# Optimization experiments

Measured on AMD Instinct MI355X. Metric: run time of the kernel, lower is better.

Reference implementation:

```python
import jax, jax.numpy as jnp
import numpy as np

N_NODES = 100000
N_EDGES = 640000
D_IN = 128
D_OUT = 128


def setup_inputs() -> dict:
    key = jax.random.key(0)
    k1, k2, k3, k4, k5 = jax.random.split(key, 5)
    feats = jax.random.normal(k1, (N_NODES, D_IN), dtype=jnp.float32)
    src = jax.random.randint(k2, (N_EDGES,), 0, N_NODES, dtype=jnp.int32)
    dst = jax.random.randint(k3, (N_EDGES,), 0, N_NODES, dtype=jnp.int32)
    # Xavier-normal-ish init (gain for relu = sqrt(2))
    std = float(np.sqrt(2.0) * np.sqrt(2.0 / (D_IN + D_OUT)))
    linear_skip_weight = jax.random.normal(k4, (D_OUT, D_IN), dtype=jnp.float32) * std
    linear_msg_weight = jax.random.normal(k5, (D_OUT, D_IN), dtype=jnp.float32) * std
    linear_skip_bias = jnp.zeros((D_OUT,), dtype=jnp.float32)
    linear_msg_bias = jnp.zeros((D_OUT,), dtype=jnp.float32)
    return {
        "feats": feats,
        "src": src,
        "dst": dst,
        "linear_skip_weight": linear_skip_weight,
        "linear_skip_bias": linear_skip_bias,
        "linear_msg_weight": linear_msg_weight,
        "linear_msg_bias": linear_msg_bias,
    }


def reference(feats, src, dst, linear_skip_weight, linear_skip_bias,
              linear_msg_weight, linear_msg_bias):
    n = feats.shape[0]
    # degree from scatter-add of edge weights (ones) at source rows
    deg = jax.ops.segment_sum(jnp.ones_like(src, dtype=feats.dtype), src,
                              num_segments=n)
    deg_inv_sqrt = jnp.where(deg > 0, jax.lax.rsqrt(jnp.maximum(deg, 1.0)) * (deg > 0), 0.0)
    deg_inv_sqrt = jnp.where(deg > 0, deg ** -0.5, 0.0)
    # normalize source features, gather along edges, scatter-sum to dst
    feat_src = feats * deg_inv_sqrt[:, None]           # [N, D_IN]
    msgs = feat_src[src]                               # [E, D_IN]
    rst = jax.ops.segment_sum(msgs, dst, num_segments=n)  # [N, D_IN]
    rst = rst * deg_inv_sqrt[:, None]
    rst_ = rst @ linear_msg_weight.T + linear_msg_bias
    skip_x = feats @ linear_skip_weight.T + linear_skip_bias
    return rst_ + skip_x
```

## Files before the change

kernel.cpp:

```cpp
#include <hip/hip_runtime.h>

#define N_NODES 100000
#define N_EDGES 640000
#define D 128
#define NB ((N_NODES + 1023) / 1024)

typedef short v8s __attribute__((ext_vector_type(8)));
typedef float v4f __attribute__((ext_vector_type(4)));

__device__ __forceinline__ unsigned short f2bf(float x) {
    unsigned int u = __builtin_bit_cast(unsigned int, x);
    u += 0x7fffu + ((u >> 16) & 1u);
    return (unsigned short)(u >> 16);
}
__device__ __forceinline__ float bf2f(unsigned int hi) {
    return __builtin_bit_cast(float, hi << 16);
}

__global__ __launch_bounds__(256) void k_zero(int4* __restrict__ pk4) {
    int i = blockIdx.x * blockDim.x + threadIdx.x;
    if (i < N_NODES / 4) pk4[i] = make_int4(0, 0, 0, 0);
}

__global__ __launch_bounds__(256) void k_pre(const float* __restrict__ feats,
                                             const float* __restrict__ Wm,
                                             const float* __restrict__ Ws,
                                             const float* __restrict__ bmsg,
                                             const float* __restrict__ bskip,
                                             const int* __restrict__ src,
                                             const int* __restrict__ dst,
                                             unsigned int* __restrict__ pk,
                                             unsigned short* __restrict__ Bcat,
                                             float* __restrict__ bias,
                                             char* __restrict__ outb) {
    int i = blockIdx.x * blockDim.x + threadIdx.x;
    if (i < D * D) {
        int j = i >> 7;
        int k = i & 127;
        Bcat[j * 256 + k]       = f2bf(Wm[i]);
        Bcat[j * 256 + 128 + k] = f2bf(Ws[i]);
    }
    if (i < D) bias[i] = bmsg[i] + bskip[i];
    if (i < N_EDGES) {
        atomicAdd(&pk[src[i]], 1u);
        atomicAdd(&pk[dst[i]], 0x10000u);
    }
    int g = i * 8;
    int row = g >> 7;
    int col = g & 127;
    if (row < N_NODES) {
        const float4* s = (const float4*)(feats + g);
        float4 x = s[0], y = s[1];
        uint4 p;
        p.x = (unsigned)f2bf(x.x) | ((unsigned)f2bf(x.y) << 16);
        p.y = (unsigned)f2bf(x.z) | ((unsigned)f2bf(x.w) << 16);
        p.z = (unsigned)f2bf(y.x) | ((unsigned)f2bf(y.y) << 16);
        p.w = (unsigned)f2bf(y.z) | ((unsigned)f2bf(y.w) << 16);
        *(uint4*)(outb + (size_t)row * 512 + 256 + col * 2) = p;
    }
}

__global__ __launch_bounds__(256) void k_scan1(const unsigned int* __restrict__ pk,
                                               int* __restrict__ rowptr,
                                               int* __restrict__ bsums) {
    __shared__ int sd[256];
    int t = threadIdx.x;
    int i0 = blockIdx.x * 1024 + t * 4;
    int v[4];
    int s = 0;
#pragma unroll
    for (int q = 0; q < 4; q++) {
        int i = i0 + q;
        v[q] = (i < N_NODES) ? (int)(pk[i] >> 16) : 0;
        s += v[q];
    }
    sd[t] = s;
    __syncthreads();
    for (int off = 1; off < 256; off <<= 1) {
        int y = (t >= off) ? sd[t - off] : 0;
        __syncthreads();
        sd[t] += y;
        __syncthreads();
    }
    int run = sd[t] - s;
    if (t == 255) bsums[blockIdx.x] = sd[255];
#pragma unroll
    for (int q = 0; q < 4; q++) {
        int i = i0 + q;
        if (i < N_NODES) rowptr[i] = run;
        run += v[q];
    }
}

__global__ __launch_bounds__(128) void k_scan2(int* __restrict__ bsums) {
    __shared__ int sd[128];
    int t = threadIdx.x;
    int v = (t < NB) ? bsums[t] : 0;
    sd[t] = v;
    __syncthreads();
    for (int off = 1; off < 128; off <<= 1) {
        int y = (t >= off) ? sd[t - off] : 0;
        __syncthreads();
        sd[t] += y;
        __syncthreads();
    }
    if (t < NB) bsums[t] = sd[t] - v;
}

__global__ __launch_bounds__(256) void k_scan3(const int* __restrict__ bsums,
                                               int* __restrict__ rowptr,
                                               const unsigned int* __restrict__ pk,
                                               float* __restrict__ dis) {
    int add = bsums[blockIdx.x];
    int i0 = blockIdx.x * 1024 + threadIdx.x * 4;
#pragma unroll
    for (int q = 0; q < 4; q++) {
        int i = i0 + q;
        if (i < N_NODES) {
            rowptr[i] += add;
            int d = (int)(pk[i] & 0xffffu);
            dis[i] = (d > 0) ? (1.0f / sqrtf((float)d)) : 0.0f;
        }
    }
}

__global__ __launch_bounds__(256) void k_fill(const int* __restrict__ src,
                                              const int* __restrict__ dst,
                                              int* __restrict__ rowptr,
                                              int* __restrict__ csr_src) {
    int e = blockIdx.x * blockDim.x + threadIdx.x;
    if (e < N_EDGES) {
        int p = atomicAdd(&rowptr[dst[e]], 1);
        csr_src[p] = src[e];
    }
}

__global__ __launch_bounds__(256) void k_agg(char* __restrict__ outb,
                                             const int* __restrict__ rowptr,
                                             const int* __restrict__ csr_src,
                                             const float* __restrict__ dis) {
    int wid = (int)((blockIdx.x * (unsigned)blockDim.x + threadIdx.x) >> 6);
    int lane = threadIdx.x & 63;
    if (wid >= N_NODES) return;
    int grp = lane >> 4;
    int sub = lane & 15;
    int start = (wid == 0) ? 0 : rowptr[wid - 1];
    int end = rowptr[wid];
    float acc[8];
#pragma unroll
    for (int i = 0; i < 8; i++) acc[i] = 0.f;

    for (int base = start; base < end; base += 4) {
        int e = base + grp;
        if (e < end) {
            int s = csr_src[e];
            float sc = dis[s];
            uint4 v = *(const uint4*)(outb + (size_t)s * 512 + 256 + sub * 16);
            acc[0] += bf2f(v.x & 0xffffu) * sc;
            acc[1] += bf2f(v.x >> 16) * sc;
            acc[2] += bf2f(v.y & 0xffffu) * sc;
            acc[3] += bf2f(v.y >> 16) * sc;
            acc[4] += bf2f(v.z & 0xffffu) * sc;
            acc[5] += bf2f(v.z >> 16) * sc;
            acc[6] += bf2f(v.w & 0xffffu) * sc;
            acc[7] += bf2f(v.w >> 16) * sc;
        }
    }
#pragma unroll
    for (int i = 0; i < 8; i++) {
        acc[i] += __shfl_xor(acc[i], 16);
        acc[i] += __shfl_xor(acc[i], 32);
    }
    if (grp == 0) {
        float scn = dis[wid];
        uint4 p;
        p.x = (unsigned)f2bf(acc[0] * scn) | ((unsigned)f2bf(acc[1] * scn) << 16);
        p.y = (unsigned)f2bf(acc[2] * scn) | ((unsigned)f2bf(acc[3] * scn) << 16);
        p.z = (unsigned)f2bf(acc[4] * scn) | ((unsigned)f2bf(acc[5] * scn) << 16);
        p.w = (unsigned)f2bf(acc[6] * scn) | ((unsigned)f2bf(acc[7] * scn) << 16);
        *(uint4*)(outb + (size_t)wid * 512 + sub * 16) = p;
    }
}

__global__ __launch_bounds__(256) void k_gemm(const unsigned short* __restrict__ Bcat,
                                              const float* __restrict__ bias,
                                              float* __restrict__ outf) {
    __shared__ unsigned short Bl[128][264];
    const char* Ab = (const char*)outf;
    int tid = threadIdx.x;
    int lane = tid & 63;
    int w = tid >> 6;
    int n0 = blockIdx.x * 128;

    for (int i = tid; i < 128 * 32; i += 256) {
        int r = i >> 5, c = i & 31;
        *(uint4*)(&Bl[r][c * 8]) = *(const uint4*)(Bcat + r * 256 + c * 8);
    }
    __syncthreads();

    int q = lane >> 4;
    int lr = lane & 15;

    int r0 = n0 + w * 32 + lr;      if (r0 > N_NODES - 1) r0 = N_NODES - 1;
    int r1 = n0 + w * 32 + 16 + lr; if (r1 > N_NODES - 1) r1 = N_NODES - 1;
    const char* a0p = Ab + (size_t)r0 * 512 + q * 16;
    const char* a1p = Ab + (size_t)r1 * 512 + q * 16;

    v4f acc[2][8];
#pragma unroll
    for (int mt = 0; mt < 2; mt++)
#pragma unroll
        for (int t = 0; t < 8; t++) acc[mt][t] = (v4f){0.f, 0.f, 0.f, 0.f};

#pragma unroll
    for (int kk = 0; kk < 8; kk++) {
        v8s a0 = *(const v8s*)(a0p + kk * 64);
        v8s a1 = *(const v8s*)(a1p + kk * 64);
#pragma unroll
        for (int t = 0; t < 8; t++) {
            v8s b = *(const v8s*)(&Bl[t * 16 + lr][kk * 32 + q * 8]);
            acc[0][t] = __builtin_amdgcn_mfma_f32_16x16x32_bf16(a0, b, acc[0][t], 0, 0, 0);
            acc[1][t] = __builtin_amdgcn_mfma_f32_16x16x32_bf16(a1, b, acc[1][t], 0, 0, 0);
        }
    }

#pragma unroll
    for (int t = 0; t < 8; t++) {
        float bv = bias[t * 16 + lr];
#pragma unroll
        for (int mt = 0; mt < 2; mt++) {
            int rowb = n0 + w * 32 + mt * 16 + q * 4;
#pragma unroll
            for (int r = 0; r < 4; r++) {
                int row = rowb + r;
                if (row < N_NODES)
                    outf[(size_t)row * 128 + t * 16 + lr] = acc[mt][t][r] + bv;
            }
        }
    }
}

extern "C" void kernel_launch(void* const* d_in, const int* in_sizes, int n_in,
                              void* d_out, int out_size, void* d_ws, size_t ws_size,
                              hipStream_t stream) {
    const float* feats = (const float*)d_in[0];
    const int*   src   = (const int*)d_in[1];
    const int*   dst   = (const int*)d_in[2];
    const float* Wskip = (const float*)d_in[3];
    const float* bskip = (const float*)d_in[4];
    const float* Wmsg  = (const float*)d_in[5];
    const float* bmsg  = (const float*)d_in[6];

    char* w = (char*)d_ws;
    unsigned int*   pk      = (unsigned int*)w;
    float*          dis     = (float*)(w + 400000);
    int*            rowptr  = (int*)(w + 800000);
    int*            bsums   = (int*)(w + 1200128);
    unsigned short* Bcat    = (unsigned short*)(w + 1200640);
    float*          bias    = (float*)(w + 1266176);
    int*            csr_src = (int*)(w + 1266688);

    hipLaunchKernelGGL(k_zero, dim3((N_NODES / 4 + 255) / 256), dim3(256), 0, stream,
                       (int4*)pk);
    hipLaunchKernelGGL(k_pre, dim3((N_NODES * (D / 8) + 255) / 256), dim3(256), 0,
                       stream, feats, Wmsg, Wskip, bmsg, bskip, src, dst, pk, Bcat,
                       bias, (char*)d_out);
    hipLaunchKernelGGL(k_scan1, dim3(NB), dim3(256), 0, stream, pk, rowptr, bsums);
    hipLaunchKernelGGL(k_scan2, dim3(1), dim3(128), 0, stream, bsums);
    hipLaunchKernelGGL(k_scan3, dim3(NB), dim3(256), 0, stream, bsums, rowptr,
                       pk, dis);
    hipLaunchKernelGGL(k_fill, dim3((N_EDGES + 255) / 256), dim3(256), 0, stream,
                       src, dst, rowptr, csr_src);
    hipLaunchKernelGGL(k_agg, dim3((N_NODES * 64 + 255) / 256), dim3(256), 0, stream,
                       (char*)d_out, rowptr, csr_src, dis);
    hipLaunchKernelGGL(k_gemm, dim3((N_NODES + 127) / 128), dim3(256), 0, stream,
                       Bcat, bias, (float*)d_out);
}
```

Measured before the change: 277.4 us.

## Replace CSR build with fixed-capacity per-node buckets filled during degree counting

When the workspace is large enough, the kernel fills a 16-slot per-destination bucket during the same atomic pass that counts degrees. Edges past 16 slots go to a global overflow list. This drops the three scan kernels and the CSR fill kernel. The source normalisation is computed on the fly with rsqrt of the packed degree instead of a precomputed array. The trade-offs: bucket writes are scattered, high-degree nodes scan the whole overflow list, and results silently drop edges if overflow exceeds the fixed cap.

```diff
diff --git a/kernel.cpp b/kernel.cpp
--- a/kernel.cpp
+++ b/kernel.cpp
@@ -4,6 +4,8 @@
 #define N_EDGES 640000
 #define D 128
 #define NB ((N_NODES + 1023) / 1024)
+#define BKT_C 16
+#define OVF_CAP 32768
 
 typedef short v8s __attribute__((ext_vector_type(8)));
 typedef float v4f __attribute__((ext_vector_type(4)));
@@ -17,9 +19,11 @@
     return __builtin_bit_cast(float, hi << 16);
 }
 
-__global__ __launch_bounds__(256) void k_zero(int4* __restrict__ pk4) {
+__global__ __launch_bounds__(256) void k_zero(int4* __restrict__ pk4,
+                                              int* __restrict__ ovf_cnt) {
     int i = blockIdx.x * blockDim.x + threadIdx.x;
     if (i < N_NODES / 4) pk4[i] = make_int4(0, 0, 0, 0);
+    if (i == 0) *ovf_cnt = 0;
 }
 
 __global__ __launch_bounds__(256) void k_pre(const float* __restrict__ feats,
@@ -32,7 +36,10 @@
                                              unsigned int* __restrict__ pk,
                                              unsigned short* __restrict__ Bcat,
                                              float* __restrict__ bias,
-                                             char* __restrict__ outb) {
+                                             char* __restrict__ outb,
+                                             int* __restrict__ bucket,
+                                             int* __restrict__ ovf_cnt,
+                                             int2* __restrict__ ovf) {
     int i = blockIdx.x * blockDim.x + threadIdx.x;
     if (i < D * D) {
         int j = i >> 7;
@@ -42,15 +49,26 @@
     }
     if (i < D) bias[i] = bmsg[i] + bskip[i];
     if (i < N_EDGES) {
-        atomicAdd(&pk[src[i]], 1u);
-        atomicAdd(&pk[dst[i]], 0x10000u);
+        int s = src[i];
+        int d = dst[i];
+        atomicAdd(&pk[s], 1u);
+        unsigned int old = atomicAdd(&pk[d], 0x10000u);
+        if (bucket) {
+            unsigned int p = old >> 16;
+            if (p < BKT_C) {
+                bucket[d * BKT_C + (int)p] = s;
+            } else {
+                int q = atomicAdd(ovf_cnt, 1);
+                if (q < OVF_CAP) ovf[q] = make_int2(d, s);
+            }
+        }
     }
     int g = i * 8;
     int row = g >> 7;
     int col = g & 127;
     if (row < N_NODES) {
-        const float4* s = (const float4*)(feats + g);
-        float4 x = s[0], y = s[1];
+        const float4* sp = (const float4*)(feats + g);
+        float4 x = sp[0], y = sp[1];
         uint4 p;
         p.x = (unsigned)f2bf(x.x) | ((unsigned)f2bf(x.y) << 16);
         p.y = (unsigned)f2bf(x.z) | ((unsigned)f2bf(x.w) << 16);
@@ -108,19 +126,13 @@
 }
 
 __global__ __launch_bounds__(256) void k_scan3(const int* __restrict__ bsums,
-                                               int* __restrict__ rowptr,
-                                               const unsigned int* __restrict__ pk,
-                                               float* __restrict__ dis) {
+                                               int* __restrict__ rowptr) {
     int add = bsums[blockIdx.x];
     int i0 = blockIdx.x * 1024 + threadIdx.x * 4;
 #pragma unroll
     for (int q = 0; q < 4; q++) {
         int i = i0 + q;
-        if (i < N_NODES) {
-            rowptr[i] += add;
-            int d = (int)(pk[i] & 0xffffu);
-            dis[i] = (d > 0) ? (1.0f / sqrtf((float)d)) : 0.0f;
-        }
+        if (i < N_NODES) rowptr[i] += add;
     }
 }
 
@@ -135,10 +147,78 @@
     }
 }
 
-__global__ __launch_bounds__(256) void k_agg(char* __restrict__ outb,
-                                             const int* __restrict__ rowptr,
-                                             const int* __restrict__ csr_src,
-                                             const float* __restrict__ dis) {
+__device__ __forceinline__ void agg_edge(const char* outb,
+                                         const unsigned int* pk,
+                                         int s, int sub, float* acc) {
+    float sc = rsqrtf((float)(pk[s] & 0xffffu));
+    uint4 v = *(const uint4*)(outb + (size_t)s * 512 + 256 + sub * 16);
+    acc[0] += bf2f(v.x & 0xffffu) * sc;
+    acc[1] += bf2f(v.x >> 16) * sc;
+    acc[2] += bf2f(v.y & 0xffffu) * sc;
+    acc[3] += bf2f(v.y >> 16) * sc;
+    acc[4] += bf2f(v.z & 0xffffu) * sc;
+    acc[5] += bf2f(v.z >> 16) * sc;
+    acc[6] += bf2f(v.w & 0xffffu) * sc;
+    acc[7] += bf2f(v.w >> 16) * sc;
+}
+
+__device__ __forceinline__ void agg_finish(char* outb, int wid,
+                                           unsigned int pkn, int grp, int sub,
+                                           float* acc) {
+#pragma unroll
+    for (int i = 0; i < 8; i++) {
+        acc[i] += __shfl_xor(acc[i], 16);
+        acc[i] += __shfl_xor(acc[i], 32);
+    }
+    if (grp == 0) {
+        int dsrc = (int)(pkn & 0xffffu);
+        float scn = (dsrc > 0) ? rsqrtf((float)dsrc) : 0.0f;
+        uint4 p;
+        p.x = (unsigned)f2bf(acc[0] * scn) | ((unsigned)f2bf(acc[1] * scn) << 16);
+        p.y = (unsigned)f2bf(acc[2] * scn) | ((unsigned)f2bf(acc[3] * scn) << 16);
+        p.z = (unsigned)f2bf(acc[4] * scn) | ((unsigned)f2bf(acc[5] * scn) << 16);
+        p.w = (unsigned)f2bf(acc[6] * scn) | ((unsigned)f2bf(acc[7] * scn) << 16);
+        *(uint4*)(outb + (size_t)wid * 512 + sub * 16) = p;
+    }
+}
+
+__global__ __launch_bounds__(256) void k_agg_bkt(char* __restrict__ outb,
+                                                 const unsigned int* __restrict__ pk,
+                                                 const int* __restrict__ bucket,
+                                                 const int* __restrict__ ovf_cnt,
+                                                 const int2* __restrict__ ovf) {
+    int wid = (int)((blockIdx.x * (unsigned)blockDim.x + threadIdx.x) >> 6);
+    int lane = threadIdx.x & 63;
+    if (wid >= N_NODES) return;
+    int grp = lane >> 4;
+    int sub = lane & 15;
+    unsigned int pkn = pk[wid];
+    int cnt = (int)(pkn >> 16);
+    int m = cnt < BKT_C ? cnt : BKT_C;
+    const int* bk = bucket + wid * BKT_C;
+    float acc[8];
+#pragma unroll
+    for (int i = 0; i < 8; i++) acc[i] = 0.f;
+
+    for (int base = 0; base < m; base += 4) {
+        int e = base + grp;
+        if (e < m) agg_edge(outb, pk, bk[e], sub, acc);
+    }
+    if (cnt > BKT_C) {
+        int no = *ovf_cnt;
+        if (no > OVF_CAP) no = OVF_CAP;
+        for (int i = grp; i < no; i += 4) {
+            int2 p = ovf[i];
+            if (p.x == wid) agg_edge(outb, pk, p.y, sub, acc);
+        }
+    }
+    agg_finish(outb, wid, pkn, grp, sub, acc);
+}
+
+__global__ __launch_bounds__(256) void k_agg_csr(char* __restrict__ outb,
+                                                 const unsigned int* __restrict__ pk,
+                                                 const int* __restrict__ rowptr,
+                                                 const int* __restrict__ csr_src) {
     int wid = (int)((blockIdx.x * (unsigned)blockDim.x + threadIdx.x) >> 6);
     int lane = threadIdx.x & 63;
     if (wid >= N_NODES) return;
@@ -149,37 +229,11 @@
     float acc[8];
 #pragma unroll
     for (int i = 0; i < 8; i++) acc[i] = 0.f;
-
     for (int base = start; base < end; base += 4) {
         int e = base + grp;
-        if (e < end) {
-            int s = csr_src[e];
-            float sc = dis[s];
-            uint4 v = *(const uint4*)(outb + (size_t)s * 512 + 256 + sub * 16);
-            acc[0] += bf2f(v.x & 0xffffu) * sc;
-            acc[1] += bf2f(v.x >> 16) * sc;
-            acc[2] += bf2f(v.y & 0xffffu) * sc;
-            acc[3] += bf2f(v.y >> 16) * sc;
-            acc[4] += bf2f(v.z & 0xffffu) * sc;
-            acc[5] += bf2f(v.z >> 16) * sc;
-            acc[6] += bf2f(v.w & 0xffffu) * sc;
-            acc[7] += bf2f(v.w >> 16) * sc;
-        }
-    }
-#pragma unroll
-    for (int i = 0; i < 8; i++) {
-        acc[i] += __shfl_xor(acc[i], 16);
-        acc[i] += __shfl_xor(acc[i], 32);
-    }
-    if (grp == 0) {
-        float scn = dis[wid];
-        uint4 p;
-        p.x = (unsigned)f2bf(acc[0] * scn) | ((unsigned)f2bf(acc[1] * scn) << 16);
-        p.y = (unsigned)f2bf(acc[2] * scn) | ((unsigned)f2bf(acc[3] * scn) << 16);
-        p.z = (unsigned)f2bf(acc[4] * scn) | ((unsigned)f2bf(acc[5] * scn) << 16);
-        p.w = (unsigned)f2bf(acc[6] * scn) | ((unsigned)f2bf(acc[7] * scn) << 16);
-        *(uint4*)(outb + (size_t)wid * 512 + sub * 16) = p;
-    }
+        if (e < end) agg_edge(outb, pk, csr_src[e], sub, acc);
+    }
+    agg_finish(outb, wid, pk[wid], grp, sub, acc);
 }
 
 __global__ __launch_bounds__(256) void k_gemm(const unsigned short* __restrict__ Bcat,
@@ -252,27 +306,49 @@
     const float* bmsg  = (const float*)d_in[6];
 
     char* w = (char*)d_ws;
-    unsigned int*   pk      = (unsigned int*)w;
-    float*          dis     = (float*)(w + 400000);
-    int*            rowptr  = (int*)(w + 800000);
-    int*            bsums   = (int*)(w + 1200128);
-    unsigned short* Bcat    = (unsigned short*)(w + 1200640);
-    float*          bias    = (float*)(w + 1266176);
-    int*            csr_src = (int*)(w + 1266688);
-
-    hipLaunchKernelGGL(k_zero, dim3((N_NODES / 4 + 255) / 256), dim3(256), 0, stream,
-                       (int4*)pk);
-    hipLaunchKernelGGL(k_pre, dim3((N_NODES * (D / 8) + 255) / 256), dim3(256), 0,
-                       stream, feats, Wmsg, Wskip, bmsg, bskip, src, dst, pk, Bcat,
-                       bias, (char*)d_out);
-    hipLaunchKernelGGL(k_scan1, dim3(NB), dim3(256), 0, stream, pk, rowptr, bsums);
-    hipLaunchKernelGGL(k_scan2, dim3(1), dim3(128), 0, stream, bsums);
-    hipLaunchKernelGGL(k_scan3, dim3(NB), dim3(256), 0, stream, bsums, rowptr,
-                       pk, dis);
-    hipLaunchKernelGGL(k_fill, dim3((N_EDGES + 255) / 256), dim3(256), 0, stream,
-                       src, dst, rowptr, csr_src);
-    hipLaunchKernelGGL(k_agg, dim3((N_NODES * 64 + 255) / 256), dim3(256), 0, stream,
-                       (char*)d_out, rowptr, csr_src, dis);
-    hipLaunchKernelGGL(k_gemm, dim3((N_NODES + 127) / 128), dim3(256), 0, stream,
-                       Bcat, bias, (float*)d_out);
-}
+
+    bool pathA = ws_size >= (size_t)7128320;
+
+    if (pathA) {
+        unsigned int*   pk      = (unsigned int*)w;
+        int*            ovf_cnt = (int*)(w + 400000);
+        unsigned short* Bcat    = (unsigned short*)(w + 400128);
+        float*          bias    = (float*)(w + 465664);
+        int*            bucket  = (int*)(w + 466176);
+        int2*           ovf     = (int2*)(w + 6866176);
+
+        hipLaunchKernelGGL(k_zero, dim3((N_NODES / 4 + 255) / 256), dim3(256), 0,
+                           stream, (int4*)pk, ovf_cnt);
+        hipLaunchKernelGGL(k_pre, dim3((N_NODES * (D / 8) + 255) / 256), dim3(256),
+                           0, stream, feats, Wmsg, Wskip, bmsg, bskip, src, dst, pk,
+                           Bcat, bias, (char*)d_out, bucket, ovf_cnt, ovf);
+        hipLaunchKernelGGL(k_agg_bkt, dim3((N_NODES * 64 + 255) / 256), dim3(256), 0,
+                           stream, (char*)d_out, pk, bucket, ovf_cnt, ovf);
+        hipLaunchKernelGGL(k_gemm, dim3((N_NODES + 127) / 128), dim3(256), 0, stream,
+                           Bcat, bias, (float*)d_out);
+    } else {
+        unsigned int*   pk      = (unsigned int*)w;
+        int*            rowptr  = (int*)(w + 400000);
+        int*            bsums   = (int*)(w + 800128);
+        unsigned short* Bcat    = (unsigned short*)(w + 800640);
+        float*          bias    = (float*)(w + 866176);
+        int*            csr_src = (int*)(w + 866688);
+
+        hipLaunchKernelGGL(k_zero, dim3((N_NODES / 4 + 255) / 256), dim3(256), 0,
+                           stream, (int4*)pk, (int*)(w + 400000) );
+        hipLaunchKernelGGL(k_pre, dim3((N_NODES * (D / 8) + 255) / 256), dim3(256),
+                           0, stream, feats, Wmsg, Wskip, bmsg, bskip, src, dst, pk,
+                           Bcat, bias, (char*)d_out, (int*)nullptr, (int*)nullptr,
+                           (int2*)nullptr);
+        hipLaunchKernelGGL(k_scan1, dim3(NB), dim3(256), 0, stream, pk, rowptr,
+                           bsums);
+        hipLaunchKernelGGL(k_scan2, dim3(1), dim3(128), 0, stream, bsums);
+        hipLaunchKernelGGL(k_scan3, dim3(NB), dim3(256), 0, stream, bsums, rowptr);
+        hipLaunchKernelGGL(k_fill, dim3((N_EDGES + 255) / 256), dim3(256), 0, stream,
+                           src, dst, rowptr, csr_src);
+        hipLaunchKernelGGL(k_agg_csr, dim3((N_NODES * 64 + 255) / 256), dim3(256), 0,
+                           stream, (char*)d_out, pk, rowptr, csr_src);
+        hipLaunchKernelGGL(k_gemm, dim3((N_NODES + 127) / 128), dim3(256), 0, stream,
+                           Bcat, bias, (float*)d_out);
+    }
+}
```

Measured after the change: 236.1 us. 1.17x faster.
